# Performance work log

Hardware: AMD Instinct MI355X
Metric: run time of the kernel (lower is better)

## Reference

```python
import jax, jax.numpy as jnp
import numpy as np

B, T, D, H = 4, 4096, 1024, 64

def setup_inputs() -> dict:
    key = jax.random.key(0)
    k1, k2, k3, k4 = jax.random.split(key, 4)
    scale = 1.0 / np.sqrt(D)
    return {
        "x": jax.random.normal(k1, (B, T, D), dtype=jnp.float32),
        "Wq": jax.random.normal(k2, (D, H), dtype=jnp.float32) * scale,
        "Wk": jax.random.normal(k3, (D, H), dtype=jnp.float32) * scale,
        "Wv": jax.random.normal(k4, (D, H), dtype=jnp.float32) * scale,
    }

def reference(x, Wq, Wk, Wv):
    # Projections (Linear without bias): [B,T,H]
    q = jnp.einsum('btd,dh->bth', x, Wq)
    k = jnp.einsum('btd,dh->bth', x, Wk)
    v = jnp.einsum('btd,dh->bth', x, Wv)
    head_size = q.shape[-1]
    # Full T x T scores, scaled by sqrt(head_size) as in the source
    attn = jnp.einsum('bqh,bkh->bqk', q, k) / jnp.sqrt(jnp.float32(head_size))
    t = x.shape[1]
    causal = jnp.tril(jnp.ones((t, t), dtype=bool))  # [T,T]
    attn = jnp.where(causal[None, :, :], attn, -jnp.inf)
    attn = jax.nn.softmax(attn, axis=-1)
    # dropout prob = 0.0 -> identity
    out = jnp.einsum('bqk,bkh->bqh', attn, v)
    return out
```

## Files before the change

kernel.cpp:

```cpp
#include <hip/hip_runtime.h>
#include <hip/hip_bf16.h>
#include <math.h>

#define BB 4
#define TT 4096
#define DD 1024
#define HH 64
#define MTOT (BB * TT)
#define NCH 4

typedef short short8 __attribute__((ext_vector_type(8)));
typedef float f32x4  __attribute__((ext_vector_type(4)));
typedef unsigned int u32;
typedef unsigned long long u64;

__device__ __forceinline__ unsigned short f2bf(float f) {
    unsigned u = __builtin_bit_cast(unsigned, f);
    unsigned r = (u + 0x7fffu + ((u >> 16) & 1u)) >> 16;
    return (unsigned short)r;
}

__device__ __forceinline__ unsigned long long pack4(float a, float b, float c, float d) {
    return (unsigned long long)f2bf(a) |
           ((unsigned long long)f2bf(b) << 16) |
           ((unsigned long long)f2bf(c) << 32) |
           ((unsigned long long)f2bf(d) << 48);
}

__device__ __forceinline__ void gl16(const void* g, void* l) {
    __builtin_amdgcn_global_load_lds(
        (const __attribute__((address_space(1))) u32*)g,
        (__attribute__((address_space(3))) u32*)l, 16, 0, 0);
}

#define QOFF  0
#define KOFF  (MTOT * HH)
#define VOFF  (2 * MTOT * HH)
#define BF_TOTAL (3 * MTOT * HH)

__global__ __launch_bounds__(256) void transpose_w(
    const float* __restrict__ Wq, const float* __restrict__ Wk,
    const float* __restrict__ Wv, unsigned short* __restrict__ Wt)
{
    const int w = blockIdx.y;
    const float* W = (w == 0) ? Wq : (w == 1) ? Wk : Wv;
    unsigned short* o = Wt + (size_t)w * 64 * 1024;
    const int t  = threadIdx.x;
    const int n4 = t & 15;
    const int k0 = blockIdx.x * 64 + (t >> 4) * 4;

    float v[4][4];
#pragma unroll
    for (int ii = 0; ii < 4; ++ii) {
        float4 r = *(const float4*)&W[(size_t)(k0 + ii) * HH + n4 * 4];
        v[ii][0] = r.x; v[ii][1] = r.y; v[ii][2] = r.z; v[ii][3] = r.w;
    }
#pragma unroll
    for (int cc = 0; cc < 4; ++cc) {
        unsigned long long pk = pack4(v[0][cc], v[1][cc], v[2][cc], v[3][cc]);
        *(unsigned long long*)&o[(size_t)(n4 * 4 + cc) * 1024 + k0] = pk;
    }
}

__global__ __launch_bounds__(256, 2) void qkv_proj(
    const float* __restrict__ x,
    const unsigned short* __restrict__ Wt,
    unsigned short* __restrict__ qkv)
{
    const int tid   = threadIdx.x;
    const int lane  = tid & 63;
    const int wave  = tid >> 6;
    const int l15   = lane & 15;
    const int quad  = lane >> 4;
    const int m0    = blockIdx.x * 32;
    const int strip = wave & 1;
    const int half  = wave >> 1;

    __shared__ float          Af[2][32 * 64];
    __shared__ unsigned short Bs[2][192 * 64];

    const int ar  = lane >> 4;
    const int as  = lane & 15;
    const int bc  = lane >> 3;
    const int bs2 = (lane & 7) ^ bc;

#define STAGEW(it, p)                                                        \
    {                                                                        \
        const int kc_ = (it) * 64;                                           \
        _Pragma("unroll")                                                    \
        for (int jj = 0; jj < 2; ++jj) {                                     \
            int j   = wave * 2 + jj;                                         \
            int row = 4 * j + ar;                                            \
            int sw  = as ^ (row & 15);                                       \
            gl16(x + (size_t)(m0 + row) * DD + kc_ + sw * 4,                 \
                 &Af[p][j * 256]);                                           \
        }                                                                    \
        _Pragma("unroll")                                                    \
        for (int jj = 0; jj < 6; ++jj) {                                     \
            int j    = wave * 6 + jj;                                        \
            int gcol = 8 * j + bc;                                           \
            gl16(Wt + (size_t)gcol * 1024 + kc_ + bs2 * 8,                   \
                 &Bs[p][j * 512]);                                           \
        }                                                                    \
    }

    f32x4 acc[6];
#pragma unroll
    for (int i = 0; i < 6; ++i) acc[i] = (f32x4){0.f, 0.f, 0.f, 0.f};

    STAGEW(0, 0)
    __syncthreads();
    int p = 0;

    for (int it = 0; it < 16; ++it) {
        if (it < 15) STAGEW(it + 1, p ^ 1)

        const int row = strip * 16 + l15;
#pragma unroll
        for (int ks = 0; ks < 2; ++ks) {
            int c0 = ks * 8 + quad * 2;
            float4 a0 = *(const float4*)&Af[p][row * 64 + ((c0)     ^ l15) * 4];
            float4 a1 = *(const float4*)&Af[p][row * 64 + ((c0 + 1) ^ l15) * 4];
            short8 af;
            {
                u32* ap = (u32*)&af;
                asm("v_cvt_pk_bf16_f32 %0, %1, %2" : "=v"(ap[0]) : "v"(a0.x), "v"(a0.y));
                asm("v_cvt_pk_bf16_f32 %0, %1, %2" : "=v"(ap[1]) : "v"(a0.z), "v"(a0.w));
                asm("v_cvt_pk_bf16_f32 %0, %1, %2" : "=v"(ap[2]) : "v"(a1.x), "v"(a1.y));
                asm("v_cvt_pk_bf16_f32 %0, %1, %2" : "=v"(ap[3]) : "v"(a1.z), "v"(a1.w));
            }
            int cb = (ks * 4 + quad) ^ (l15 & 7);
#pragma unroll
            for (int jj = 0; jj < 6; ++jj) {
                int col = (half * 6 + jj) * 16 + l15;
                short8 bfr = *(const short8*)&Bs[p][col * 64 + cb * 8];
                acc[jj] = __builtin_amdgcn_mfma_f32_16x16x32_bf16(af, bfr, acc[jj], 0, 0, 0);
            }
        }
        __syncthreads();
        p ^= 1;
    }
#undef STAGEW

    const float QS = 0.125f * 1.44269504088896f;
    unsigned short* q_bf  = qkv + QOFF;
    unsigned short* k_bf  = qkv + KOFF;
    unsigned short* vt_bf = qkv + VOFF;
#pragma unroll
    for (int jj = 0; jj < 6; ++jj) {
        int g = half * 6 + jj, w = g >> 2, col = (g & 3) * 16 + l15;
#pragma unroll
        for (int r = 0; r < 4; ++r) {
            int m = m0 + strip * 16 + quad * 4 + r;
            float val = acc[jj][r];
            if (w == 0) val *= QS;
            unsigned short bv = f2bf(val);
            if (w == 0)      q_bf[(size_t)m * HH + col] = bv;
            else if (w == 1) k_bf[(size_t)m * HH + col] = bv;
            else {
                int b = m >> 12, t = m & 4095;
                vt_bf[(size_t)b * HH * TT + (size_t)col * TT + t] = bv;
            }
        }
    }
}

__global__ __launch_bounds__(256, 3) void flash_attn(
    const unsigned short* __restrict__ qkv,
    float* __restrict__ Opart,
    float* __restrict__ Mpart,
    float* __restrict__ Lpart)
{
    const int qt = 63 - blockIdx.x;
    const int b  = blockIdx.y;
    const int c  = blockIdx.z;
    if (c * 16 > qt) return;
    const int j0   = c * 16;
    const int jmax = min(j0 + 16, qt + 1);

    const int tid  = threadIdx.x;
    const int lane = tid & 63;
    const int wave = tid >> 6;
    const int l15  = lane & 15;
    const int quad = lane >> 4;

    const unsigned short* q_g  = qkv + QOFF + (size_t)b * TT * HH;
    const unsigned short* k_g  = qkv + KOFF + (size_t)b * TT * HH;
    const unsigned short* vt_g = qkv + VOFF + (size_t)b * HH * TT;

    __shared__ unsigned short Ks[2][128 * 64];
    __shared__ unsigned short Vs[64 * 128];

    const int kr3 = lane >> 3;
    const int kch = lane & 7;
    const int vr2 = lane >> 4;
    const int vch = lane & 15;

#define STAGE_K(jr_, p_)                                                      \
    {                                                                         \
        const unsigned short* kp = k_g + (size_t)(jr_) * 64 * HH;             \
        _Pragma("unroll")                                                     \
        for (int i = 0; i < 4; ++i) {                                         \
            int g = wave * 4 + i;                                             \
            gl16(kp + (size_t)(g * 8 + kr3) * HH + (kch ^ kr3) * 8,           \
                 &Ks[p_][g * 512]);                                           \
        }                                                                     \
    }
#define STAGE_V(jr_)                                                          \
    {                                                                         \
        const unsigned short* vp = vt_g + (size_t)(jr_) * 64;                 \
        _Pragma("unroll")                                                     \
        for (int i = 0; i < 4; ++i) {                                         \
            int g = wave * 4 + i;                                             \
            int h = g * 4 + vr2;                                              \
            gl16(vp + (size_t)h * TT + (vch ^ ((h >> 1) & 7)) * 8,            \
                 &Vs[g * 512]);                                               \
        }                                                                     \
    }

    short8 qf[2];
#pragma unroll
    for (int kk = 0; kk < 2; ++kk)
        qf[kk] = *(const short8*)&q_g[(size_t)(qt * 64 + wave * 16 + l15) * HH + kk * 32 + quad * 8];

    f32x4 ov[4];
#pragma unroll
    for (int i = 0; i < 4; ++i) ov[i] = (f32x4){0.f, 0.f, 0.f, 0.f};
    float m_run = -1e30f, l_run = 0.f;

    STAGE_K(j0, 0)
    __syncthreads();
    int p = 0;

    const int swv = 2 * ((l15 >> 1) & 7);

    for (int jr = j0; jr < jmax; jr += 2) {
        const bool two = (jmax - jr) >= 2;

        STAGE_V(jr)
        if (jr + 2 < jmax) STAGE_K(jr + 2, p ^ 1)

        f32x4 st0[4], st1[4];
#pragma unroll
        for (int i = 0; i < 4; ++i) {
            st0[i] = (f32x4){0.f, 0.f, 0.f, 0.f};
            st1[i] = (f32x4){0.f, 0.f, 0.f, 0.f};
        }
        __builtin_amdgcn_s_setprio(1);
#pragma unroll
        for (int kk = 0; kk < 2; ++kk)
#pragma unroll
            for (int mt = 0; mt < 4; ++mt) {
                short8 a = *(const short8*)&Ks[p][(mt * 16 + l15) * 64 +
                                                  (((kk * 4 + quad) ^ (l15 & 7)) * 8)];
                st0[mt] = __builtin_amdgcn_mfma_f32_16x16x32_bf16(a, qf[kk], st0[mt], 0, 0, 0);
            }
        if (two) {
#pragma unroll
            for (int kk = 0; kk < 2; ++kk)
#pragma unroll
                for (int mt = 0; mt < 4; ++mt) {
                    short8 a = *(const short8*)&Ks[p][(64 + mt * 16 + l15) * 64 +
                                                      (((kk * 4 + quad) ^ (l15 & 7)) * 8)];
                    st1[mt] = __builtin_amdgcn_mfma_f32_16x16x32_bf16(a, qf[kk], st1[mt], 0, 0, 0);
                }
        }
        __builtin_amdgcn_s_setprio(0);

        const int qg = wave * 16 + l15;
        if (jr == qt) {
#pragma unroll
            for (int mt = 0; mt < 4; ++mt)
#pragma unroll
                for (int r = 0; r < 4; ++r)
                    if (mt * 16 + quad * 4 + r > qg) st0[mt][r] = -1e30f;
        } else if (two && jr + 1 == qt) {
#pragma unroll
            for (int mt = 0; mt < 4; ++mt)
#pragma unroll
                for (int r = 0; r < 4; ++r)
                    if (mt * 16 + quad * 4 + r > qg) st1[mt][r] = -1e30f;
        }

        float mloc = -1e30f;
#pragma unroll
        for (int mt = 0; mt < 4; ++mt)
#pragma unroll
            for (int r = 0; r < 4; ++r) mloc = fmaxf(mloc, st0[mt][r]);
        if (two) {
#pragma unroll
            for (int mt = 0; mt < 4; ++mt)
#pragma unroll
                for (int r = 0; r < 4; ++r) mloc = fmaxf(mloc, st1[mt][r]);
        }
        mloc = fmaxf(mloc, __shfl_xor(mloc, 16));
        mloc = fmaxf(mloc, __shfl_xor(mloc, 32));

        if (!__all(mloc <= m_run)) {
            const float m_new = fmaxf(m_run, mloc);
            const float alpha = exp2f(m_run - m_new);
            m_run = m_new;
            l_run *= alpha;
            float a0 = __shfl(alpha, quad * 4 + 0);
            float a1 = __shfl(alpha, quad * 4 + 1);
            float a2 = __shfl(alpha, quad * 4 + 2);
            float a3 = __shfl(alpha, quad * 4 + 3);
#pragma unroll
            for (int ht = 0; ht < 4; ++ht) {
                ov[ht][0] *= a0; ov[ht][1] *= a1;
                ov[ht][2] *= a2; ov[ht][3] *= a3;
            }
        }

        float ssum = 0.f;
#pragma unroll
        for (int mt = 0; mt < 4; ++mt)
#pragma unroll
            for (int r = 0; r < 4; ++r) {
                float pv = exp2f(st0[mt][r] - m_run);
                st0[mt][r] = pv; ssum += pv;
            }
        if (two) {
#pragma unroll
            for (int mt = 0; mt < 4; ++mt)
#pragma unroll
                for (int r = 0; r < 4; ++r) {
                    float pv = exp2f(st1[mt][r] - m_run);
                    st1[mt][r] = pv; ssum += pv;
                }
        }
        ssum += __shfl_xor(ssum, 16);
        ssum += __shfl_xor(ssum, 32);
        l_run += ssum;

        short8 pa00, pa01, pa10, pa11;
        {
            u32* pp = (u32*)&pa00;
            asm("v_cvt_pk_bf16_f32 %0, %1, %2" : "=v"(pp[0]) : "v"(st0[0][0]), "v"(st0[0][1]));
            asm("v_cvt_pk_bf16_f32 %0, %1, %2" : "=v"(pp[1]) : "v"(st0[0][2]), "v"(st0[0][3]));
            asm("v_cvt_pk_bf16_f32 %0, %1, %2" : "=v"(pp[2]) : "v"(st0[1][0]), "v"(st0[1][1]));
            asm("v_cvt_pk_bf16_f32 %0, %1, %2" : "=v"(pp[3]) : "v"(st0[1][2]), "v"(st0[1][3]));
            pp = (u32*)&pa01;
            asm("v_cvt_pk_bf16_f32 %0, %1, %2" : "=v"(pp[0]) : "v"(st0[2][0]), "v"(st0[2][1]));
            asm("v_cvt_pk_bf16_f32 %0, %1, %2" : "=v"(pp[1]) : "v"(st0[2][2]), "v"(st0[2][3]));
            asm("v_cvt_pk_bf16_f32 %0, %1, %2" : "=v"(pp[2]) : "v"(st0[3][0]), "v"(st0[3][1]));
            asm("v_cvt_pk_bf16_f32 %0, %1, %2" : "=v"(pp[3]) : "v"(st0[3][2]), "v"(st0[3][3]));
        }
        if (two) {
            u32* pp = (u32*)&pa10;
            asm("v_cvt_pk_bf16_f32 %0, %1, %2" : "=v"(pp[0]) : "v"(st1[0][0]), "v"(st1[0][1]));
            asm("v_cvt_pk_bf16_f32 %0, %1, %2" : "=v"(pp[1]) : "v"(st1[0][2]), "v"(st1[0][3]));
            asm("v_cvt_pk_bf16_f32 %0, %1, %2" : "=v"(pp[2]) : "v"(st1[1][0]), "v"(st1[1][1]));
            asm("v_cvt_pk_bf16_f32 %0, %1, %2" : "=v"(pp[3]) : "v"(st1[1][2]), "v"(st1[1][3]));
            pp = (u32*)&pa11;
            asm("v_cvt_pk_bf16_f32 %0, %1, %2" : "=v"(pp[0]) : "v"(st1[2][0]), "v"(st1[2][1]));
            asm("v_cvt_pk_bf16_f32 %0, %1, %2" : "=v"(pp[1]) : "v"(st1[2][2]), "v"(st1[2][3]));
            asm("v_cvt_pk_bf16_f32 %0, %1, %2" : "=v"(pp[2]) : "v"(st1[3][0]), "v"(st1[3][1]));
            asm("v_cvt_pk_bf16_f32 %0, %1, %2" : "=v"(pp[3]) : "v"(st1[3][2]), "v"(st1[3][3]));
        }

        __syncthreads();

        __builtin_amdgcn_s_setprio(1);
#pragma unroll
        for (int kk = 0; kk < 2; ++kk) {
            short8 a = kk ? pa01 : pa00;
            int c8 = kk * 8 + quad;
#pragma unroll
            for (int ht = 0; ht < 4; ++ht) {
                int rb = (ht * 16 + l15) * 128;
                u64 lo = *(const u64*)&Vs[rb + ((c8 ^ swv) << 2)];
                u64 hi = *(const u64*)&Vs[rb + ((c8 ^ 4 ^ swv) << 2)];
                short8 vb;
                ((u64*)&vb)[0] = lo;
                ((u64*)&vb)[1] = hi;
                ov[ht] = __builtin_amdgcn_mfma_f32_16x16x32_bf16(a, vb, ov[ht], 0, 0, 0);
            }
        }
        if (two) {
#pragma unroll
            for (int kk = 0; kk < 2; ++kk) {
                short8 a = kk ? pa11 : pa10;
                int c8 = 16 + kk * 8 + quad;
#pragma unroll
                for (int ht = 0; ht < 4; ++ht) {
                    int rb = (ht * 16 + l15) * 128;
                    u64 lo = *(const u64*)&Vs[rb + ((c8 ^ swv) << 2)];
                    u64 hi = *(const u64*)&Vs[rb + ((c8 ^ 4 ^ swv) << 2)];
                    short8 vb;
                    ((u64*)&vb)[0] = lo;
                    ((u64*)&vb)[1] = hi;
                    ov[ht] = __builtin_amdgcn_mfma_f32_16x16x32_bf16(a, vb, ov[ht], 0, 0, 0);
                }
            }
        }
        __builtin_amdgcn_s_setprio(0);

        __syncthreads();
        p ^= 1;
    }
#undef STAGE_K
#undef STAGE_V

    float* Ob = Opart + ((size_t)((b * 64 + qt) * NCH + c)) * 4096;
#pragma unroll
    for (int ht = 0; ht < 4; ++ht)
#pragma unroll
        for (int r = 0; r < 4; ++r)
            Ob[(size_t)(wave * 16 + quad * 4 + r) * HH + ht * 16 + l15] = ov[ht][r];
    if (quad == 0) {
        size_t mi = (size_t)((b * 64 + qt) * NCH + c) * 64 + wave * 16 + l15;
        Mpart[mi] = m_run;
        Lpart[mi] = l_run;
    }
}

__global__ __launch_bounds__(256) void combine(
    const float* __restrict__ Opart,
    const float* __restrict__ Mpart,
    const float* __restrict__ Lpart,
    float* __restrict__ out)
{
    const int qt = blockIdx.x;
    const int b  = blockIdx.y;
    const int nc = (qt >> 4) + 1;
    const int t  = threadIdx.x;
    const int row = t >> 2;
    const int seg = t & 3;

    const size_t base = (size_t)(b * 64 + qt) * NCH;

    float M = -1e30f;
    for (int c = 0; c < nc; ++c)
        M = fmaxf(M, Mpart[(base + c) * 64 + row]);

    float L = 0.f;
    f32x4 o[4];
#pragma unroll
    for (int i = 0; i < 4; ++i) o[i] = (f32x4){0.f, 0.f, 0.f, 0.f};
    for (int c = 0; c < nc; ++c) {
        float w = exp2f(Mpart[(base + c) * 64 + row] - M);
        L += w * Lpart[(base + c) * 64 + row];
        const float* Ob = Opart + (base + c) * 4096 + (size_t)row * HH + seg * 16;
#pragma unroll
        for (int i = 0; i < 4; ++i) {
            f32x4 v = *(const f32x4*)(Ob + i * 4);
            o[i] += v * w;
        }
    }
    float invL = 1.0f / L;
    float* op = out + ((size_t)b * TT + qt * 64 + row) * HH + seg * 16;
#pragma unroll
    for (int i = 0; i < 4; ++i)
        *(f32x4*)(op + i * 4) = o[i] * invL;
}

extern "C" void kernel_launch(void* const* d_in, const int* in_sizes, int n_in,
                              void* d_out, int out_size, void* d_ws, size_t ws_size,
                              hipStream_t stream) {
    const float* x  = (const float*)d_in[0];
    const float* Wq = (const float*)d_in[1];
    const float* Wk = (const float*)d_in[2];
    const float* Wv = (const float*)d_in[3];
    float* out = (float*)d_out;

    unsigned short* qkv = (unsigned short*)d_ws;
    float* Opart = (float*)((char*)d_ws + BF_TOTAL * 2);
    float* Mpart = Opart + (size_t)BB * 64 * NCH * 4096;
    float* Lpart = Mpart + (size_t)BB * 64 * NCH * 64;

    unsigned short* Wt = (unsigned short*)d_out;

    transpose_w<<<dim3(16, 3), 256, 0, stream>>>(Wq, Wk, Wv, Wt);
    qkv_proj<<<dim3(MTOT / 32), 256, 0, stream>>>(x, Wt, qkv);
    flash_attn<<<dim3(64, BB, NCH), 256, 0, stream>>>(qkv, Opart, Mpart, Lpart);
    combine<<<dim3(64, BB), 256, 0, stream>>>(Opart, Mpart, Lpart, out);
}
```

Before: 152.6 us.

## Pair adjacent query tiles per 512-thread block to share K/V staging

Each flash-attention block now handles two adjacent query tiles with 8 waves, so one K/V tile staged in shared memory is reused by both query tiles and each wave issues half as many loads. The KV split count doubles to 8 chunks of 8 tiles with a flattened 1D grid, and the variable-length 'two' branch is removed so every iteration processes two KV tiles unconditionally, masking the extra tile fully for the lower query tile. The intent is to halve K/V staging traffic per query and shorten the tail with finer splits. In exchange the combine step has more partials to merge, workspace use grows, and some masked work is wasted on diagonal tiles.

```diff
diff --git a/kernel.cpp b/kernel.cpp
--- a/kernel.cpp
+++ b/kernel.cpp
@@ -7,7 +7,7 @@
 #define DD 1024
 #define HH 64
 #define MTOT (BB * TT)
-#define NCH 4
+#define NCH 8
 
 typedef short short8 __attribute__((ext_vector_type(8)));
 typedef float f32x4  __attribute__((ext_vector_type(4)));
@@ -165,22 +165,28 @@
     }
 }
 
-__global__ __launch_bounds__(256, 3) void flash_attn(
+__global__ __launch_bounds__(512, 4) void flash_attn(
     const unsigned short* __restrict__ qkv,
     float* __restrict__ Opart,
     float* __restrict__ Mpart,
     float* __restrict__ Lpart)
 {
-    const int qt = 63 - blockIdx.x;
-    const int b  = blockIdx.y;
-    const int c  = blockIdx.z;
-    if (c * 16 > qt) return;
-    const int j0   = c * 16;
-    const int jmax = min(j0 + 16, qt + 1);
+    const int id  = blockIdx.x;
+    const int pr  = id >> 5;
+    const int rem = id & 31;
+    const int c   = rem >> 2;
+    const int b   = rem & 3;
+    const int qtB = 63 - 2 * pr;
+    const int qtA = qtB - 1;
+    if (c * 8 > qtB) return;
+    const int j0   = c * 8;
+    const int jmax = min(j0 + 8, qtB + 1);
 
     const int tid  = threadIdx.x;
     const int lane = tid & 63;
     const int wave = tid >> 6;
+    const int wv   = wave & 3;
+    const int qt   = (wave >> 2) ? qtB : qtA;
     const int l15  = lane & 15;
     const int quad = lane >> 4;
 
@@ -200,8 +206,8 @@
     {                                                                         \
         const unsigned short* kp = k_g + (size_t)(jr_) * 64 * HH;             \
         _Pragma("unroll")                                                     \
-        for (int i = 0; i < 4; ++i) {                                         \
-            int g = wave * 4 + i;                                             \
+        for (int i = 0; i < 2; ++i) {                                         \
+            int g = wave * 2 + i;                                             \
             gl16(kp + (size_t)(g * 8 + kr3) * HH + (kch ^ kr3) * 8,           \
                  &Ks[p_][g * 512]);                                           \
         }                                                                     \
@@ -210,8 +216,8 @@
     {                                                                         \
         const unsigned short* vp = vt_g + (size_t)(jr_) * 64;                 \
         _Pragma("unroll")                                                     \
-        for (int i = 0; i < 4; ++i) {                                         \
-            int g = wave * 4 + i;                                             \
+        for (int i = 0; i < 2; ++i) {                                         \
+            int g = wave * 2 + i;                                             \
             int h = g * 4 + vr2;                                              \
             gl16(vp + (size_t)h * TT + (vch ^ ((h >> 1) & 7)) * 8,            \
                  &Vs[g * 512]);                                               \
@@ -221,7 +227,7 @@
     short8 qf[2];
 #pragma unroll
     for (int kk = 0; kk < 2; ++kk)
-        qf[kk] = *(const short8*)&q_g[(size_t)(qt * 64 + wave * 16 + l15) * HH + kk * 32 + quad * 8];
+        qf[kk] = *(const short8*)&q_g[(size_t)(qt * 64 + wv * 16 + l15) * HH + kk * 32 + quad * 8];
 
     f32x4 ov[4];
 #pragma unroll
@@ -235,7 +241,6 @@
     const int swv = 2 * ((l15 >> 1) & 7);
 
     for (int jr = j0; jr < jmax; jr += 2) {
-        const bool two = (jmax - jr) >= 2;
 
         STAGE_V(jr)
         if (jr + 2 < jmax) STAGE_K(jr + 2, p ^ 1)
@@ -255,26 +260,26 @@
                                                   (((kk * 4 + quad) ^ (l15 & 7)) * 8)];
                 st0[mt] = __builtin_amdgcn_mfma_f32_16x16x32_bf16(a, qf[kk], st0[mt], 0, 0, 0);
             }
-        if (two) {
-#pragma unroll
-            for (int kk = 0; kk < 2; ++kk)
-#pragma unroll
-                for (int mt = 0; mt < 4; ++mt) {
-                    short8 a = *(const short8*)&Ks[p][(64 + mt * 16 + l15) * 64 +
-                                                      (((kk * 4 + quad) ^ (l15 & 7)) * 8)];
-                    st1[mt] = __builtin_amdgcn_mfma_f32_16x16x32_bf16(a, qf[kk], st1[mt], 0, 0, 0);
+#pragma unroll
+        for (int kk = 0; kk < 2; ++kk)
+#pragma unroll
+            for (int mt = 0; mt < 4; ++mt) {
+                short8 a = *(const short8*)&Ks[p][(64 + mt * 16 + l15) * 64 +
+                                                  (((kk * 4 + quad) ^ (l15 & 7)) * 8)];
+                st1[mt] = __builtin_amdgcn_mfma_f32_16x16x32_bf16(a, qf[kk], st1[mt], 0, 0, 0);
+            }
+        __builtin_amdgcn_s_setprio(0);
+
+        const int qg = wv * 16 + l15;
+        if (jr == qt) {
+#pragma unroll
+            for (int mt = 0; mt < 4; ++mt)
+#pragma unroll
+                for (int r = 0; r < 4; ++r) {
+                    if (mt * 16 + quad * 4 + r > qg) st0[mt][r] = -1e30f;
+                    st1[mt][r] = -1e30f;
                 }
-        }
-        __builtin_amdgcn_s_setprio(0);
-
-        const int qg = wave * 16 + l15;
-        if (jr == qt) {
-#pragma unroll
-            for (int mt = 0; mt < 4; ++mt)
-#pragma unroll
-                for (int r = 0; r < 4; ++r)
-                    if (mt * 16 + quad * 4 + r > qg) st0[mt][r] = -1e30f;
-        } else if (two && jr + 1 == qt) {
+        } else if (jr + 1 == qt) {
 #pragma unroll
             for (int mt = 0; mt < 4; ++mt)
 #pragma unroll
@@ -286,13 +291,10 @@
 #pragma unroll
         for (int mt = 0; mt < 4; ++mt)
 #pragma unroll
-            for (int r = 0; r < 4; ++r) mloc = fmaxf(mloc, st0[mt][r]);
-        if (two) {
-#pragma unroll
-            for (int mt = 0; mt < 4; ++mt)
-#pragma unroll
-                for (int r = 0; r < 4; ++r) mloc = fmaxf(mloc, st1[mt][r]);
-        }
+            for (int r = 0; r < 4; ++r) {
+                mloc = fmaxf(mloc, st0[mt][r]);
+                mloc = fmaxf(mloc, st1[mt][r]);
+            }
         mloc = fmaxf(mloc, __shfl_xor(mloc, 16));
         mloc = fmaxf(mloc, __shfl_xor(mloc, 32));
 
@@ -317,18 +319,11 @@
         for (int mt = 0; mt < 4; ++mt)
 #pragma unroll
             for (int r = 0; r < 4; ++r) {
-                float pv = exp2f(st0[mt][r] - m_run);
-                st0[mt][r] = pv; ssum += pv;
-            }
-        if (two) {
-#pragma unroll
-            for (int mt = 0; mt < 4; ++mt)
-#pragma unroll
-                for (int r = 0; r < 4; ++r) {
-                    float pv = exp2f(st1[mt][r] - m_run);
-                    st1[mt][r] = pv; ssum += pv;
-                }
-        }
+                float p0 = exp2f(st0[mt][r] - m_run);
+                float p1 = exp2f(st1[mt][r] - m_run);
+                st0[mt][r] = p0; st1[mt][r] = p1;
+                ssum += p0 + p1;
+            }
         ssum += __shfl_xor(ssum, 16);
         ssum += __shfl_xor(ssum, 32);
         l_run += ssum;
@@ -345,9 +340,7 @@
             asm("v_cvt_pk_bf16_f32 %0, %1, %2" : "=v"(pp[1]) : "v"(st0[2][2]), "v"(st0[2][3]));
             asm("v_cvt_pk_bf16_f32 %0, %1, %2" : "=v"(pp[2]) : "v"(st0[3][0]), "v"(st0[3][1]));
             asm("v_cvt_pk_bf16_f32 %0, %1, %2" : "=v"(pp[3]) : "v"(st0[3][2]), "v"(st0[3][3]));
-        }
-        if (two) {
-            u32* pp = (u32*)&pa10;
+            pp = (u32*)&pa10;
             asm("v_cvt_pk_bf16_f32 %0, %1, %2" : "=v"(pp[0]) : "v"(st1[0][0]), "v"(st1[0][1]));
             asm("v_cvt_pk_bf16_f32 %0, %1, %2" : "=v"(pp[1]) : "v"(st1[0][2]), "v"(st1[0][3]));
             asm("v_cvt_pk_bf16_f32 %0, %1, %2" : "=v"(pp[2]) : "v"(st1[1][0]), "v"(st1[1][1]));
@@ -377,21 +370,19 @@
                 ov[ht] = __builtin_amdgcn_mfma_f32_16x16x32_bf16(a, vb, ov[ht], 0, 0, 0);
             }
         }
-        if (two) {
-#pragma unroll
-            for (int kk = 0; kk < 2; ++kk) {
-                short8 a = kk ? pa11 : pa10;
-                int c8 = 16 + kk * 8 + quad;
-#pragma unroll
-                for (int ht = 0; ht < 4; ++ht) {
-                    int rb = (ht * 16 + l15) * 128;
-                    u64 lo = *(const u64*)&Vs[rb + ((c8 ^ swv) << 2)];
-                    u64 hi = *(const u64*)&Vs[rb + ((c8 ^ 4 ^ swv) << 2)];
-                    short8 vb;
-                    ((u64*)&vb)[0] = lo;
-                    ((u64*)&vb)[1] = hi;
-                    ov[ht] = __builtin_amdgcn_mfma_f32_16x16x32_bf16(a, vb, ov[ht], 0, 0, 0);
-                }
+#pragma unroll
+        for (int kk = 0; kk < 2; ++kk) {
+            short8 a = kk ? pa11 : pa10;
+            int c8 = 16 + kk * 8 + quad;
+#pragma unroll
+            for (int ht = 0; ht < 4; ++ht) {
+                int rb = (ht * 16 + l15) * 128;
+                u64 lo = *(const u64*)&Vs[rb + ((c8 ^ swv) << 2)];
+                u64 hi = *(const u64*)&Vs[rb + ((c8 ^ 4 ^ swv) << 2)];
+                short8 vb;
+                ((u64*)&vb)[0] = lo;
+                ((u64*)&vb)[1] = hi;
+                ov[ht] = __builtin_amdgcn_mfma_f32_16x16x32_bf16(a, vb, ov[ht], 0, 0, 0);
             }
         }
         __builtin_amdgcn_s_setprio(0);
@@ -407,9 +398,9 @@
     for (int ht = 0; ht < 4; ++ht)
 #pragma unroll
         for (int r = 0; r < 4; ++r)
-            Ob[(size_t)(wave * 16 + quad * 4 + r) * HH + ht * 16 + l15] = ov[ht][r];
+            Ob[(size_t)(wv * 16 + quad * 4 + r) * HH + ht * 16 + l15] = ov[ht][r];
     if (quad == 0) {
-        size_t mi = (size_t)((b * 64 + qt) * NCH + c) * 64 + wave * 16 + l15;
+        size_t mi = (size_t)((b * 64 + qt) * NCH + c) * 64 + wv * 16 + l15;
         Mpart[mi] = m_run;
         Lpart[mi] = l_run;
     }
@@ -423,7 +414,7 @@
 {
     const int qt = blockIdx.x;
     const int b  = blockIdx.y;
-    const int nc = (qt >> 4) + 1;
+    const int nc = (qt >> 3) + 1;
     const int t  = threadIdx.x;
     const int row = t >> 2;
     const int seg = t & 3;
@@ -473,6 +464,6 @@
 
     transpose_w<<<dim3(16, 3), 256, 0, stream>>>(Wq, Wk, Wv, Wt);
     qkv_proj<<<dim3(MTOT / 32), 256, 0, stream>>>(x, Wt, qkv);
-    flash_attn<<<dim3(64, BB, NCH), 256, 0, stream>>>(qkv, Opart, Mpart, Lpart);
+    flash_attn<<<dim3(1024), 512, 0, stream>>>(qkv, Opart, Mpart, Lpart);
     combine<<<dim3(64, BB), 256, 0, stream>>>(Opart, Mpart, Lpart, out);
 }
```

After: 163.7 us. 7.3% more time.
